# Performance work log

Hardware: AMD Instinct MI355X
Metric: run time of the kernel (lower is better)

Reference implementation:

```python
import jax, jax.numpy as jnp
import numpy as np

B_, L_, DM, DI, DS, DTR, DC = 1, 2048, 2048, 4096, 16, 128, 4


def setup_inputs() -> dict:
    key = jax.random.key(0)
    ks = jax.random.split(key, 8)
    s = lambda k, shape, scale: jax.random.normal(k, shape, jnp.float32) * scale
    inp = {
        "hidden_states": s(ks[0], (B_, L_, DM), 1.0),
        "in_proj_weight": s(ks[1], (2 * DI, DM), DM ** -0.5),
        "conv1d_weight": s(ks[2], (DI, 1, DC), DC ** -0.5),
        "x_proj_weight": s(ks[3], (DTR + 2 * DS, DI), DI ** -0.5),
        "dt_proj_weight": s(ks[4], (DI, DTR), DTR ** -0.5),
        "out_proj_weight": s(ks[5], (DM, DI), DI ** -0.5),
    }
    # dt_proj_bias = inverse-softplus of dt ~ LogUniform[1e-3, 0.1] (as in init_dtprojbias)
    dt = jnp.exp(jax.random.uniform(ks[6], (DI,), jnp.float32) * (np.log(0.1) - np.log(0.001)) + np.log(0.001))
    dt = jnp.clip(dt, 1e-4, None)
    inp["dt_proj_bias"] = dt + jnp.log(-jnp.expm1(-dt))
    # A_log init: log of repeat(arange(1, d_state+1)) per d_inner row
    inp["A_log"] = jnp.log(jnp.tile(jnp.arange(1, DS + 1, dtype=jnp.float32), (DI, 1)))
    inp["D"] = jnp.ones((DI,), jnp.float32)
    return inp


def reference(hidden_states, in_proj_weight, conv1d_weight, x_proj_weight,
              dt_proj_weight, dt_proj_bias, A_log, D, out_proj_weight):
    b, l, dm = hidden_states.shape
    di, ds = A_log.shape
    # in_proj: [b,l,dm] -> xz [b, 2*di, l]
    xz = jnp.einsum('ed,bld->bel', in_proj_weight, hidden_states)
    x, z = xz[:, :di], xz[:, di:]
    # depthwise causal conv1d (pad left d_conv-1, no bias) + SiLU
    x = jax.lax.conv_general_dilated(
        x, conv1d_weight, window_strides=(1,), padding=[(DC - 1, 0)],
        dimension_numbers=('NCH', 'OIH', 'NCH'), feature_group_count=di)
    x = jax.nn.silu(x)  # [b, di, l]
    # x_proj -> dt, B, C
    x_dbl = jnp.einsum('pd,bdl->blp', x_proj_weight, x)  # [b,l,dtr+2*ds]
    dt, Bc, Cc = jnp.split(x_dbl, [DTR, DTR + ds], axis=-1)
    delta = jnp.einsum('dr,blr->bld', dt_proj_weight, dt) + dt_proj_bias
    delta = jax.nn.softplus(delta)  # delta_softplus=True, delta_bias applied
    A = -jnp.exp(A_log)  # [di, ds]
    u = jnp.transpose(x, (0, 2, 1))  # [b,l,di]

    def step(h, inputs):
        d_t, B_t, C_t, u_t = inputs  # [b,di],[b,ds],[b,ds],[b,di]
        dA = jnp.exp(d_t[..., None] * A)                      # [b,di,ds]
        h = h * dA + (d_t * u_t)[..., None] * B_t[:, None, :]  # [b,di,ds]
        y = jnp.einsum('bdn,bn->bd', h, C_t)
        return h, y

    h0 = jnp.zeros((b, di, ds), hidden_states.dtype)
    xs = (jnp.swapaxes(delta, 0, 1), jnp.swapaxes(Bc, 0, 1),
          jnp.swapaxes(Cc, 0, 1), jnp.swapaxes(u, 0, 1))
    _, ys = jax.lax.scan(step, h0, xs)          # [l,b,di]
    y = jnp.swapaxes(ys, 0, 1) + u * D          # skip term u*D
    y = y * jax.nn.silu(jnp.transpose(z, (0, 2, 1)))  # gate
    return jnp.einsum('md,bld->blm', out_proj_weight, y)
```

## Files before the change

kernel.cpp:

```cpp
#include <hip/hip_runtime.h>
#include <hip/hip_bf16.h>

#define LSEQ 2048
#define DMODEL 2048
#define DINNER 4096
#define DSTATE 16
#define DTRANK 128
#define DCONV 4
#define DXP (DTRANK + 2*DSTATE)
#define NCHUNK 64
#define LCHUNK (LSEQ / NCHUNK)
#define KSPLIT 16
#define OKS 4

using bf16 = __hip_bfloat16;
typedef __attribute__((ext_vector_type(8))) short short8;
typedef __attribute__((ext_vector_type(4))) float float4v;

__device__ __forceinline__ float b2f(bf16 v) { return __bfloat162float(v); }
__device__ __forceinline__ bf16 f2b(float v) { return __float2bfloat16(v); }
__device__ __forceinline__ float bl16(unsigned u) { return __uint_as_float(u << 16); }
__device__ __forceinline__ float bh16(unsigned u) { return __uint_as_float(u & 0xffff0000u); }

__device__ __forceinline__ short f2bs(float v) {
    bf16 b = __float2bfloat16(v);
    union { bf16 b; short s; } u; u.b = b; return u.s;
}

__device__ __forceinline__ float fsilu(float x) {
    return x * __builtin_amdgcn_rcpf(1.0f + __expf(-x));
}

__device__ __forceinline__ short8 ld8(const float* p) {
    float4v f0 = *(const float4v*)p;
    float4v f1 = *(const float4v*)(p + 4);
    short8 r;
    r[0] = f2bs(f0[0]); r[1] = f2bs(f0[1]); r[2] = f2bs(f0[2]); r[3] = f2bs(f0[3]);
    r[4] = f2bs(f1[0]); r[5] = f2bs(f1[1]); r[6] = f2bs(f1[2]); r[7] = f2bs(f1[3]);
    return r;
}
__device__ __forceinline__ short8 ld8(const bf16* p) { return *(const short8*)p; }

template<typename CT> __device__ __forceinline__ CT cvtC(float v);
template<> __device__ __forceinline__ bf16  cvtC<bf16>(float v)  { return f2b(v); }
template<> __device__ __forceinline__ float cvtC<float>(float v) { return v; }

template<typename T> __device__ __forceinline__ float cvtL(T v);
template<> __device__ __forceinline__ float cvtL<bf16>(bf16 v)   { return b2f(v); }
template<> __device__ __forceinline__ float cvtL<float>(float v) { return v; }

__device__ __forceinline__ void glds16(const bf16* g, void* lds_base) {
    __builtin_amdgcn_global_load_lds(
        (const __attribute__((address_space(1))) void*)g,
        (__attribute__((address_space(3))) void*)lds_base, 16, 0, 0);
}

__global__ __launch_bounds__(256) void cvt4(
    const float* __restrict__ s0, bf16* __restrict__ d0, int n0,
    const float* __restrict__ s1, bf16* __restrict__ d1, int n1,
    const float* __restrict__ s2, bf16* __restrict__ d2, int n2,
    const float* __restrict__ s3, bf16* __restrict__ d3, int n3)
{
    const int b = blockIdx.x;
    const int nb0 = n0 >> 11, nb1 = n1 >> 11, nb2 = n2 >> 11;
    const float* s; bf16* d; int i;
    if (b < nb0)                  { s = s0; d = d0; i = b * 2048; }
    else if (b < nb0 + nb1)       { s = s1; d = d1; i = (b - nb0) * 2048; }
    else if (b < nb0 + nb1 + nb2) { s = s2; d = d2; i = (b - nb0 - nb1) * 2048; }
    else                          { s = s3; d = d3; i = (b - nb0 - nb1 - nb2) * 2048; }
    i += threadIdx.x * 8;
    *(short8*)(d + i) = ld8(s + i);
}

__global__ __launch_bounds__(256) void cvt1(
    const float* __restrict__ src, bf16* __restrict__ dst, int n)
{
    int i = (blockIdx.x * 256 + threadIdx.x) * 8;
    if (i >= n) return;
    *(short8*)(dst + i) = ld8(src + i);
}

#define GBAR  __builtin_amdgcn_s_barrier()
#define VMW4  asm volatile("s_waitcnt vmcnt(4)" ::: "memory")
#define VMW0  asm volatile("s_waitcnt vmcnt(0)" ::: "memory")

#define LDA8(BASE, RB, AF) do {                                                \
  _Pragma("unroll") for (int mi_ = 0; mi_ < 4; ++mi_)                          \
  _Pragma("unroll") for (int kk_ = 0; kk_ < 2; ++kk_)                          \
    AF[mi_][kk_] = *(const short8*)((BASE) + (((RB) + mi_*16 + t16) << 6)      \
                                    + ((((kk_*4) + quad) ^ sw7) << 3));        \
} while (0)

#define LDB4(BASE, RB, BF) do {                                                \
  _Pragma("unroll") for (int nj_ = 0; nj_ < 2; ++nj_)                          \
  _Pragma("unroll") for (int kk_ = 0; kk_ < 2; ++kk_)                          \
    BF[nj_][kk_] = *(const short8*)((BASE) + (((RB) + nj_*16 + t16) << 6)      \
                                    + ((((kk_*4) + quad) ^ sw7) << 3));        \
} while (0)

#define MM16(AF, BF, MO, NO) do {                                              \
  _Pragma("unroll") for (int kk_ = 0; kk_ < 2; ++kk_)                          \
  _Pragma("unroll") for (int mi_ = 0; mi_ < 4; ++mi_)                          \
  _Pragma("unroll") for (int nj_ = 0; nj_ < 2; ++nj_)                          \
    acc[(MO)+mi_][(NO)+nj_] = __builtin_amdgcn_mfma_f32_16x16x32_bf16(         \
        AF[mi_][kk_], BF[nj_][kk_], acc[(MO)+mi_][(NO)+nj_], 0, 0, 0);         \
} while (0)

#define ST_ALO(tau) do { size_t ko_ = (size_t)(tau) << 6; int bo_ = ((tau)&1) << 15; \
  glds16(sA +       ko_, dA0 + bo_);                                           \
  glds16(sA + oA1 + ko_, dA1 + bo_); } while (0)
#define ST_AHI(tau) do { size_t ko_ = (size_t)(tau) << 6; int bo_ = ((tau)&1) << 15; \
  glds16(sA + oA2 + ko_, dA2 + bo_);                                           \
  glds16(sA + oA3 + ko_, dA3 + bo_); } while (0)
#define ST_BLO(tau) do { size_t ko_ = (size_t)(tau) << 6; int bo_ = ((tau)&1) << 15; \
  glds16(sB +       ko_, dB0 + bo_);                                           \
  glds16(sB + oB1 + ko_, dB1 + bo_); } while (0)
#define ST_BHI(tau) do { size_t ko_ = (size_t)(tau) << 6; int bo_ = ((tau)&1) << 15; \
  glds16(sB + oB2 + ko_, dB2 + bo_);                                           \
  glds16(sB + oB3 + ko_, dB3 + bo_); } while (0)

#define KSTEP(T, BI) do {                                                      \
    const bf16* Ab = As[BI];                                                   \
    const bf16* Bb = Bs[BI];                                                   \
    short8 af[4][2], b0[2][2], b1[2][2];                                       \
                                       \
    LDA8(Ab, wm, af);                                                          \
    LDB4(Bb, wn, b0);                                                          \
    if ((T) + 1 < NT) { ST_AHI((T) + 1); ST_BLO((T) + 1); }                    \
    __builtin_amdgcn_s_setprio(1); MM16(af, b0, 0, 0);                         \
    __builtin_amdgcn_s_setprio(0); GBAR;                                       \
                    \
    LDB4(Bb, wn + 32, b1);                                                     \
    if ((T) + 2 < NT) ST_ALO((T) + 2);                                         \
    __builtin_amdgcn_s_setprio(1); MM16(af, b1, 0, 2);                         \
    __builtin_amdgcn_s_setprio(0); GBAR;                                       \
                           \
    LDA8(Ab, wm + 64, af);                                                     \
    if ((T) + 2 < NT) ST_BHI((T) + 2);                                         \
    __builtin_amdgcn_s_setprio(1); MM16(af, b1, 4, 2);                         \
    __builtin_amdgcn_s_setprio(0); GBAR;                                       \
                                   \
    __builtin_amdgcn_s_setprio(1); MM16(af, b0, 4, 0);                         \
    __builtin_amdgcn_s_setprio(0);                                             \
    if ((T) + 2 < NT) { VMW4; } else { VMW0; }                                 \
    GBAR;                                                                      \
} while (0)

#define GEMM_PRO_COMMON                                                        \
    const int t    = threadIdx.x;                                              \
    const int wave = t >> 6;                                                   \
    const int lane = t & 63;                                                   \
    const int t16  = lane & 15;                                                \
    const int quad = lane >> 4;                                                \
    const int sw7  = t16 & 7;                                                  \
    const int wm   = (wave >> 2) * 128;                                        \
    const int wn   = (wave & 3) * 64;                                          \
    const int lrow  = lane >> 3;                                               \
    const int lseg  = lane & 7;                                                \
    const int segx  = (lseg ^ lrow) * 8;                                       \
    const int bwoff = (wave & 3) * 8 + (wave >> 2) * 64;

#define GEMM_LDS_DSTS                                                          \
    char* dA0 = (char*)&As[0][(  0 + wave * 8) * 64];                          \
    char* dA1 = (char*)&As[0][(128 + wave * 8) * 64];                          \
    char* dA2 = (char*)&As[0][( 64 + wave * 8) * 64];                          \
    char* dA3 = (char*)&As[0][(192 + wave * 8) * 64];                          \
    char* dB0 = (char*)&Bs[0][(  0 + bwoff) * 64];                             \
    char* dB1 = (char*)&Bs[0][(128 + bwoff) * 64];                             \
    char* dB2 = (char*)&Bs[0][( 32 + bwoff) * 64];                             \
    char* dB3 = (char*)&Bs[0][(160 + bwoff) * 64];

__global__ __launch_bounds__(512, 2) void gemm_inproj(
    const bf16* __restrict__ A, int lda,
    const bf16* __restrict__ B, int ldb,
    bf16* __restrict__ C, int ldc, int K)
{
    __shared__ __align__(16) bf16 As[2][256 * 64];
    __shared__ __align__(16) bf16 Bs[2][256 * 64];
    GEMM_PRO_COMMON
    const int bid = blockIdx.x;
    const int s   = (bid & 7) * (gridDim.x >> 3) + (bid >> 3);
    const int bm0 = (s & 7) << 8;
    const int bn0 = (s >> 3) << 8;

    const bf16* sA = A + (size_t)(bm0 + wave * 8 + lrow) * lda + segx;
    const bf16* sB = B + (size_t)(bn0 + bwoff + lrow) * ldb + segx;
    const size_t oA1 = (size_t)128 * lda, oA2 = (size_t)64 * lda, oA3 = (size_t)192 * lda;
    const size_t oB1 = (size_t)128 * ldb, oB2 = (size_t)32 * ldb, oB3 = (size_t)160 * ldb;
    GEMM_LDS_DSTS

    const int NT = K >> 6;

    float4v acc[8][4];
#pragma unroll
    for (int i = 0; i < 8; ++i)
#pragma unroll
        for (int j = 0; j < 4; ++j) acc[i][j] = (float4v)(0.0f);

    ST_ALO(0); ST_AHI(0); ST_BLO(0); ST_BHI(0);
    if (NT > 1) { ST_ALO(1); ST_BHI(1); VMW4; } else { VMW0; }
    GBAR;

    for (int T = 0; T < NT; T += 2) {
        KSTEP(T, 0);
        KSTEP(T + 1, 1);
    }

#pragma unroll
    for (int mi = 0; mi < 8; ++mi) {
#pragma unroll
        for (int nj = 0; nj < 4; ++nj) {
            const int m_base = bm0 + wm + (mi >> 2) * 64 + (mi & 3) * 16 + quad * 4;
            const int n_g    = bn0 + wn + (nj >> 1) * 32 + (nj & 1) * 16 + t16;
#pragma unroll
            for (int r = 0; r < 4; ++r)
                C[(size_t)(m_base + r) * ldc + n_g] = f2b(acc[mi][nj][r]);
        }
    }
}

__global__ __launch_bounds__(512, 2) void gemm_outproj(
    const bf16* __restrict__ A, int lda,
    const bf16* __restrict__ B, int ldb,
    float* __restrict__ P, int ldc, int Kc)
{
    __shared__ __align__(16) bf16 As[2][256 * 64];
    __shared__ __align__(16) bf16 Bs[2][256 * 64];
    GEMM_PRO_COMMON
    const int bid = blockIdx.x;
    const int s   = (bid & 7) * (gridDim.x >> 3) + (bid >> 3);
    const int bm0 = (s & 7) << 8;
    const int t2  = s >> 3;
    const int bn0 = (t2 & 7) << 8;
    const int ks  = t2 >> 3;

    const bf16* sA = A + (size_t)(bm0 + wave * 8 + lrow) * lda + segx + (size_t)ks * Kc;
    const bf16* sB = B + (size_t)(bn0 + bwoff + lrow) * ldb + segx + (size_t)ks * Kc;
    const size_t oA1 = (size_t)128 * lda, oA2 = (size_t)64 * lda, oA3 = (size_t)192 * lda;
    const size_t oB1 = (size_t)128 * ldb, oB2 = (size_t)32 * ldb, oB3 = (size_t)160 * ldb;
    GEMM_LDS_DSTS

    const int NT = Kc >> 6;

    float4v acc[8][4];
#pragma unroll
    for (int i = 0; i < 8; ++i)
#pragma unroll
        for (int j = 0; j < 4; ++j) acc[i][j] = (float4v)(0.0f);

    ST_ALO(0); ST_AHI(0); ST_BLO(0); ST_BHI(0);
    if (NT > 1) { ST_ALO(1); ST_BHI(1); VMW4; } else { VMW0; }
    GBAR;

    for (int T = 0; T < NT; T += 2) {
        KSTEP(T, 0);
        KSTEP(T + 1, 1);
    }

    float* Pk = P + (size_t)ks * 2048 * (size_t)ldc;
#pragma unroll
    for (int mi = 0; mi < 8; ++mi) {
#pragma unroll
        for (int nj = 0; nj < 4; ++nj) {
            const int m_base = bm0 + wm + (mi >> 2) * 64 + (mi & 3) * 16 + quad * 4;
            const int n_g    = bn0 + wn + (nj >> 1) * 32 + (nj & 1) * 16 + t16;
#pragma unroll
            for (int r = 0; r < 4; ++r)
                Pk[(size_t)(m_base + r) * ldc + n_g] = acc[mi][nj][r];
        }
    }
}

__global__ __launch_bounds__(256) void reduce4f(
    const float* __restrict__ P, float* __restrict__ out, int MN)
{
    int i = (blockIdx.x * 256 + threadIdx.x) * 4;
    if (i >= MN) return;
    float4v s = *(const float4v*)(P + i);
#pragma unroll
    for (int ks = 1; ks < OKS; ++ks) {
        float4v v = *(const float4v*)(P + (size_t)ks * MN + i);
#pragma unroll
        for (int j = 0; j < 4; ++j) s[j] += v[j];
    }
    *(float4v*)(out + i) = s;
}

__global__ __launch_bounds__(256) void gemm_xproj(
    const bf16* __restrict__ A, int lda,
    const bf16* __restrict__ B, int ldb,
    float* __restrict__ P)
{
    __shared__ bf16 As[128][64];
    __shared__ bf16 Bs[160][64];

    const int t    = threadIdx.x;
    const int wave = t >> 6;
    const int lane = t & 63;
    const int t16  = lane & 15;
    const int quad = lane >> 4;
    const int wm   = (wave >> 1) * 64;
    const int wn   = (wave & 1) * 80;
    const int bm0  = blockIdx.x * 128;
    const int kbeg = blockIdx.y * (DINNER / KSPLIT);

    const int lrow = lane >> 3;
    const int gseg = ((lane & 7) ^ lrow) * 8;

    const bf16* Ag[4]; char* Ad[4];
#pragma unroll
    for (int g = 0; g < 4; g++) {
        int r = wave * 32 + g * 8;
        Ag[g] = A + (size_t)(bm0 + r + lrow) * lda + gseg + kbeg;
        Ad[g] = (char*)As + r * 128;
    }
    const bf16* Bg[5]; char* Bd[5];
#pragma unroll
    for (int g = 0; g < 5; g++) {
        int r = wave * 40 + g * 8;
        Bg[g] = B + (size_t)(r + lrow) * ldb + gseg + kbeg;
        Bd[g] = (char*)Bs + r * 128;
    }

    float4v acc[4][5];
#pragma unroll
    for (int i = 0; i < 4; i++)
#pragma unroll
        for (int j = 0; j < 5; j++) acc[i][j] = (float4v)(0.0f);

    const int sw = t16 & 7;

    for (int k0 = 0; k0 < DINNER / KSPLIT; k0 += 64) {
        __syncthreads();
#pragma unroll
        for (int g = 0; g < 4; g++) glds16(Ag[g] + k0, Ad[g]);
#pragma unroll
        for (int g = 0; g < 5; g++) glds16(Bg[g] + k0, Bd[g]);
        __syncthreads();

#pragma unroll
        for (int kk = 0; kk < 2; kk++) {
            const int kso = ((kk * 4 + quad) ^ sw) * 8;
            short8 a[4], b[5];
#pragma unroll
            for (int mi = 0; mi < 4; mi++)
                a[mi] = *(const short8*)(&As[wm + mi * 16 + t16][kso]);
#pragma unroll
            for (int nj = 0; nj < 5; nj++)
                b[nj] = *(const short8*)(&Bs[wn + nj * 16 + t16][kso]);
#pragma unroll
            for (int mi = 0; mi < 4; mi++)
#pragma unroll
                for (int nj = 0; nj < 5; nj++)
                    acc[mi][nj] = __builtin_amdgcn_mfma_f32_16x16x32_bf16(
                        a[mi], b[nj], acc[mi][nj], 0, 0, 0);
        }
    }

    float* Pk = P + (size_t)blockIdx.y * LSEQ * DXP;
#pragma unroll
    for (int mi = 0; mi < 4; mi++) {
#pragma unroll
        for (int nj = 0; nj < 5; nj++) {
            int n_g = wn + nj * 16 + t16;
#pragma unroll
            for (int r = 0; r < 4; r++) {
                int m_g = bm0 + wm + mi * 16 + quad * 4 + r;
                Pk[(size_t)m_g * DXP + n_g] = acc[mi][nj][r];
            }
        }
    }
}

template<int BN, typename CT, bool SP>
__global__ __launch_bounds__(256) void gemm_glds64(
    const bf16* __restrict__ A, int lda,
    const bf16* __restrict__ B, int ldb,
    CT* __restrict__ C, int ldc,
    int K, const float* __restrict__ bias)
{
    constexpr int NJ  = BN / 32;
    constexpr int BGL = BN / 32;
    __shared__ bf16 As[128][64];
    __shared__ bf16 Bs[BN][64];

    const int t    = threadIdx.x;
    const int wave = t >> 6;
    const int lane = t & 63;
    const int t16  = lane & 15;
    const int quad = lane >> 4;
    const int wm   = (wave >> 1) * 64;
    const int wn   = (wave & 1) * (BN / 2);
    const int bm0  = blockIdx.x * 128;
    const int bn0  = blockIdx.y * BN;

    const int lrow = lane >> 3;
    const int gseg = (((lane & 7) ^ lrow) * 8);

    const bf16* Ag[4]; char* Ad[4];
#pragma unroll
    for (int g = 0; g < 4; g++) {
        Ag[g] = A + (size_t)(bm0 + wave * 32 + g * 8 + lrow) * lda + gseg;
        Ad[g] = (char*)As + (wave * 32 + g * 8) * 128;
    }
    const bf16* Bg[BGL]; char* Bd[BGL];
#pragma unroll
    for (int g = 0; g < BGL; g++) {
        int r = (BN == 128) ? (wave * 32 + g * 8) : (wave * 16 + g * 8);
        Bg[g] = B + (size_t)(bn0 + r + lrow) * ldb + gseg;
        Bd[g] = (char*)Bs + r * 128;
    }

    float4v acc[4][NJ];
#pragma unroll
    for (int i = 0; i < 4; i++)
#pragma unroll
        for (int j = 0; j < NJ; j++) acc[i][j] = (float4v)(0.0f);

    const int sw = t16 & 7;

    for (int k0 = 0; k0 < K; k0 += 64) {
        __syncthreads();
#pragma unroll
        for (int g = 0; g < 4; g++)   glds16(Ag[g] + k0, Ad[g]);
#pragma unroll
        for (int g = 0; g < BGL; g++) glds16(Bg[g] + k0, Bd[g]);
        __syncthreads();

#pragma unroll
        for (int kk = 0; kk < 2; kk++) {
            const int kso = ((kk * 4 + quad) ^ sw) * 8;
            short8 a[4], b[NJ];
#pragma unroll
            for (int mi = 0; mi < 4; mi++)
                a[mi] = *(const short8*)(&As[wm + mi * 16 + t16][kso]);
#pragma unroll
            for (int nj = 0; nj < NJ; nj++)
                b[nj] = *(const short8*)(&Bs[wn + nj * 16 + t16][kso]);
#pragma unroll
            for (int mi = 0; mi < 4; mi++)
#pragma unroll
                for (int nj = 0; nj < NJ; nj++)
                    acc[mi][nj] = __builtin_amdgcn_mfma_f32_16x16x32_bf16(
                        a[mi], b[nj], acc[mi][nj], 0, 0, 0);
        }
    }

#pragma unroll
    for (int mi = 0; mi < 4; mi++) {
#pragma unroll
        for (int nj = 0; nj < NJ; nj++) {
            int n_g = bn0 + wn + nj * 16 + t16;
            float bia = SP ? bias[n_g] : 0.0f;
#pragma unroll
            for (int r = 0; r < 4; r++) {
                int m_g = bm0 + wm + mi * 16 + quad * 4 + r;
                float v = acc[mi][nj][r];
                if (SP) {
                    float x = v + bia;
                    v = (x > 20.0f) ? x : __logf(1.0f + __expf(x));
                }
                C[(size_t)m_g * ldc + n_g] = cvtC<CT>(v);
            }
        }
    }
}

template<typename AT, typename CT, bool SP>
__global__ __launch_bounds__(256) void gemm_bt(
    const AT* __restrict__ A, int lda,
    const float* __restrict__ B, int ldb,
    CT* __restrict__ C, int ldc,
    int M, int N, int K,
    const float* __restrict__ bias)
{
    __shared__ bf16 As[64][40];
    __shared__ bf16 Bs[64][40];

    const int t    = threadIdx.x;
    const int bm0  = blockIdx.x * 64;
    const int bn0  = blockIdx.y * 64;
    const int row  = t >> 2;
    const int seg  = (t & 3) * 8;
    const int wave = t >> 6;
    const int lane = t & 63;
    const int wm   = (wave >> 1) * 32;
    const int wn   = (wave & 1) * 32;
    const int t16  = lane & 15;
    const int quad = lane >> 4;

    float4v acc[2][2];
#pragma unroll
    for (int i = 0; i < 2; i++)
#pragma unroll
        for (int j = 0; j < 2; j++) acc[i][j] = (float4v)(0.0f);

    const AT*    Aptr = A + (size_t)(bm0 + row) * lda + seg;
    const float* Bptr = B + (size_t)(bn0 + row) * ldb + seg;
    const bool a_ok = (bm0 + row) < M;
    const bool b_ok = (bn0 + row) < N;
    const short8 zero8 = (short8)(0);

    for (int k0 = 0; k0 < K; k0 += 32) {
        short8 av = a_ok ? ld8(Aptr + k0) : zero8;
        short8 bv = b_ok ? ld8(Bptr + k0) : zero8;
        __syncthreads();
        *(short8*)(&As[row][seg]) = av;
        *(short8*)(&Bs[row][seg]) = bv;
        __syncthreads();

        short8 a0 = *(const short8*)(&As[wm + t16][quad * 8]);
        short8 a1 = *(const short8*)(&As[wm + 16 + t16][quad * 8]);
        short8 b0 = *(const short8*)(&Bs[wn + t16][quad * 8]);
        short8 b1 = *(const short8*)(&Bs[wn + 16 + t16][quad * 8]);
        acc[0][0] = __builtin_amdgcn_mfma_f32_16x16x32_bf16(a0, b0, acc[0][0], 0, 0, 0);
        acc[0][1] = __builtin_amdgcn_mfma_f32_16x16x32_bf16(a0, b1, acc[0][1], 0, 0, 0);
        acc[1][0] = __builtin_amdgcn_mfma_f32_16x16x32_bf16(a1, b0, acc[1][0], 0, 0, 0);
        acc[1][1] = __builtin_amdgcn_mfma_f32_16x16x32_bf16(a1, b1, acc[1][1], 0, 0, 0);
    }

#pragma unroll
    for (int i = 0; i < 2; i++) {
#pragma unroll
        for (int j = 0; j < 2; j++) {
            int n_g = bn0 + wn + j * 16 + t16;
            if (n_g >= N) continue;
            float bia = SP ? bias[n_g] : 0.0f;
#pragma unroll
            for (int r = 0; r < 4; r++) {
                int m_g = bm0 + wm + i * 16 + quad * 4 + r;
                if (m_g >= M) continue;
                float v = acc[i][j][r];
                if (SP) {
                    float x = v + bia;
                    v = (x > 20.0f) ? x : log1pf(__expf(x));
                }
                C[(size_t)m_g * ldc + n_g] = cvtC<CT>(v);
            }
        }
    }
}

__global__ __launch_bounds__(256) void reduce_splitk(
    const float* __restrict__ P, bf16* __restrict__ C, float* __restrict__ bc, int MN)
{
    int i = blockIdx.x * 256 + threadIdx.x;
    if (i >= MN) return;
    float s = 0.f;
#pragma unroll
    for (int ks = 0; ks < KSPLIT; ks++) s += P[(size_t)ks * MN + i];
    C[i] = f2b(s);
    int l = i / DXP;
    int p = i - l * DXP;
    if (p >= DTRANK) bc[l * 32 + (p - DTRANK)] = s;
}

__global__ __launch_bounds__(256) void conv_silu_par(
    const bf16* __restrict__ xz, const float* __restrict__ w, bf16* __restrict__ xc)
{
    const int d  = blockIdx.x * 256 + threadIdx.x;
    const int lc = blockIdx.y * 64;
    const float w0 = w[d * 4 + 0];
    const float w1 = w[d * 4 + 1];
    const float w2 = w[d * 4 + 2];
    const float w3 = w[d * 4 + 3];
    const size_t S = 2 * DINNER;
    const bf16* p = xz + d;
    float xm3 = 0.f, xm2 = 0.f, xm1 = 0.f;
    if (lc >= 3) {
        xm3 = b2f(p[(size_t)(lc - 3) * S]);
        xm2 = b2f(p[(size_t)(lc - 2) * S]);
        xm1 = b2f(p[(size_t)(lc - 1) * S]);
    }
    for (int l = lc; l < lc + 64; ++l) {
        float x0 = b2f(p[(size_t)l * S]);
        float a = w0 * xm3 + w1 * xm2 + w2 * xm1 + w3 * x0;
        xc[(size_t)l * DINNER + d] = f2b(fsilu(a));
        xm3 = xm2; xm2 = xm1; xm1 = x0;
    }
}

__global__ __launch_bounds__(256) void conv_silu_inplace(
    bf16* __restrict__ xz, const float* __restrict__ w)
{
    const int d = blockIdx.x * 256 + threadIdx.x;
    const float w0 = w[d * 4 + 0];
    const float w1 = w[d * 4 + 1];
    const float w2 = w[d * 4 + 2];
    const float w3 = w[d * 4 + 3];
    bf16* p = xz + d;
    const size_t S = 2 * DINNER;
    float xm3 = 0.f, xm2 = 0.f, xm1 = 0.f;
    for (int l = 0; l < LSEQ; l += 4) {
        float x0 = b2f(p[(size_t)(l + 0) * S]);
        float x1 = b2f(p[(size_t)(l + 1) * S]);
        float x2 = b2f(p[(size_t)(l + 2) * S]);
        float x3 = b2f(p[(size_t)(l + 3) * S]);
        float a0 = w0 * xm3 + w1 * xm2 + w2 * xm1 + w3 * x0;
        float a1 = w0 * xm2 + w1 * xm1 + w2 * x0  + w3 * x1;
        float a2 = w0 * xm1 + w1 * x0  + w2 * x1  + w3 * x2;
        float a3 = w0 * x0  + w1 * x1  + w2 * x2  + w3 * x3;
        p[(size_t)(l + 0) * S] = f2b(a0 / (1.0f + __expf(-a0)));
        p[(size_t)(l + 1) * S] = f2b(a1 / (1.0f + __expf(-a1)));
        p[(size_t)(l + 2) * S] = f2b(a2 / (1.0f + __expf(-a2)));
        p[(size_t)(l + 3) * S] = f2b(a3 / (1.0f + __expf(-a3)));
        xm3 = x1; xm2 = x2; xm1 = x3;
    }
}

__global__ __launch_bounds__(256) void scan_chunk1(
    const float* __restrict__ dlt, const bf16* __restrict__ xc,
    const float* __restrict__ bc, const float* __restrict__ A_log,
    float* __restrict__ hend, float* __restrict__ Pbuf)
{
    const int d = blockIdx.x * 256 + threadIdx.x;
    const int c = blockIdx.y;

    float Ac[16];
    {
        const float* ap = A_log + d * DSTATE;
#pragma unroll
        for (int i = 0; i < 16; i++) Ac[i] = -__expf(ap[i]);
    }

    float h[16];
#pragma unroll
    for (int i = 0; i < 16; i++) h[i] = 0.f;
    float sdelta = 0.f;

    const float* pd = dlt + (size_t)c * LCHUNK * DINNER + d;
    const bf16*  pu = xc  + (size_t)c * LCHUNK * DINNER + d;
    const float* pb = bc  + (size_t)c * LCHUNK * 32;

#pragma unroll 2
    for (int l = 0; l < LCHUNK; ++l) {
        const float delta = *pd;
        const float u     = b2f(*pu);
        const float du    = delta * u;
        sdelta += delta;
        float4v B0 = *(const float4v*)pb;
        float4v B1 = *(const float4v*)(pb + 4);
        float4v B2 = *(const float4v*)(pb + 8);
        float4v B3 = *(const float4v*)(pb + 12);
#pragma unroll
        for (int i = 0; i < 16; i++) {
            float dA = __expf(delta * Ac[i]);
            float Bi = (i < 4) ? B0[i] : (i < 8) ? B1[i - 4] : (i < 12) ? B2[i - 8] : B3[i - 12];
            h[i] = h[i] * dA + du * Bi;
        }
        pd += DINNER; pu += DINNER; pb += 32;
    }

    float* hp = hend + ((size_t)c * DINNER + d) * DSTATE;
    float* pp = Pbuf + ((size_t)c * DINNER + d) * DSTATE;
#pragma unroll
    for (int q = 0; q < 4; q++) {
        float4v hv, pv;
#pragma unroll
        for (int j = 0; j < 4; j++) {
            hv[j] = h[q * 4 + j];
            pv[j] = __expf(sdelta * Ac[q * 4 + j]);
        }
        *(float4v*)(hp + q * 4) = hv;
        *(float4v*)(pp + q * 4) = pv;
    }
}

__global__ __launch_bounds__(256) void scan_combine(
    float* __restrict__ hend, const float* __restrict__ Pbuf)
{
    const int dn = blockIdx.x * 256 + threadIdx.x;
    const size_t STR = (size_t)DINNER * DSTATE;
    float H = 0.f;
    size_t idx = dn;
    for (int c0 = 0; c0 < NCHUNK; c0 += 8) {
        float he[8], pp[8];
#pragma unroll
        for (int j = 0; j < 8; j++) {
            he[j] = hend[idx + (size_t)j * STR];
            pp[j] = Pbuf[idx + (size_t)j * STR];
        }
#pragma unroll
        for (int j = 0; j < 8; j++) {
            hend[idx + (size_t)j * STR] = H;
            H = he[j] + pp[j] * H;
        }
        idx += 8 * STR;
    }
}

__global__ __launch_bounds__(256) void scan_chunk2(
    const float* __restrict__ dlt, const bf16* __restrict__ xc,
    bf16* __restrict__ xz, const float* __restrict__ bc,
    const float* __restrict__ A_log, const float* __restrict__ Dp,
    const float* __restrict__ Hin)
{
    const int d = blockIdx.x * 256 + threadIdx.x;
    const int c = blockIdx.y;

    float Ac[16];
    {
        const float* ap = A_log + d * DSTATE;
#pragma unroll
        for (int i = 0; i < 16; i++) Ac[i] = -__expf(ap[i]);
    }
    const float Dv = Dp[d];

    float h[16];
    {
        const float* hp = Hin + ((size_t)c * DINNER + d) * DSTATE;
#pragma unroll
        for (int q = 0; q < 4; q++) {
            float4v hv = *(const float4v*)(hp + q * 4);
#pragma unroll
            for (int j = 0; j < 4; j++) h[q * 4 + j] = hv[j];
        }
    }

    const float* pd = dlt + (size_t)c * LCHUNK * DINNER + d;
    const bf16*  pu = xc  + (size_t)c * LCHUNK * DINNER + d;
    const float* pb = bc  + (size_t)c * LCHUNK * 32;
    bf16*        pz = xz  + (size_t)c * LCHUNK * (2 * DINNER) + DINNER + d;

#pragma unroll 2
    for (int l = 0; l < LCHUNK; ++l) {
        const float delta = *pd;
        const float u     = b2f(*pu);
        const float du    = delta * u;
        float4v B0 = *(const float4v*)pb;
        float4v B1 = *(const float4v*)(pb + 4);
        float4v B2 = *(const float4v*)(pb + 8);
        float4v B3 = *(const float4v*)(pb + 12);
        float4v C0 = *(const float4v*)(pb + 16);
        float4v C1 = *(const float4v*)(pb + 20);
        float4v C2 = *(const float4v*)(pb + 24);
        float4v C3 = *(const float4v*)(pb + 28);
        float yv = 0.f;
#pragma unroll
        for (int i = 0; i < 16; i++) {
            float dA = __expf(delta * Ac[i]);
            float Bi = (i < 4) ? B0[i] : (i < 8) ? B1[i - 4] : (i < 12) ? B2[i - 8] : B3[i - 12];
            float Ci = (i < 4) ? C0[i] : (i < 8) ? C1[i - 4] : (i < 12) ? C2[i - 8] : C3[i - 12];
            h[i] = h[i] * dA + du * Bi;
            yv += h[i] * Ci;
        }
        yv += u * Dv;
        float z = b2f(*pz);
        yv *= fsilu(z);
        *pz = f2b(yv);
        pd += DINNER; pu += DINNER; pb += 32; pz += 2 * DINNER;
    }
}

template<typename DT>
__global__ __launch_bounds__(256) void scan_serial(
    const DT* __restrict__ dlt, bf16* __restrict__ xz,
    const bf16* __restrict__ xdbl,
    const float* __restrict__ A_log, const float* __restrict__ Dp)
{
    const int nq = threadIdx.x & 3;
    const int d  = blockIdx.x * 64 + (threadIdx.x >> 2);
    float Ac[4];
#pragma unroll
    for (int i = 0; i < 4; i++)
        Ac[i] = -__expf(A_log[d * DSTATE + nq * 4 + i]);
    const float Dv = Dp[d];
    float h[4] = {0.f, 0.f, 0.f, 0.f};
    for (int l = 0; l < LSEQ; ++l) {
        const float delta = cvtL<DT>(dlt[(size_t)l * DINNER + d]);
        const float u     = b2f(xz[(size_t)l * (2 * DINNER) + d]);
        const uint2 qb = *(const uint2*)(xdbl + (size_t)l * DXP + DTRANK + nq * 4);
        const uint2 qc = *(const uint2*)(xdbl + (size_t)l * DXP + DTRANK + DSTATE + nq * 4);
        float Bv[4] = { bl16(qb.x), bh16(qb.x), bl16(qb.y), bh16(qb.y) };
        float Cv[4] = { bl16(qc.x), bh16(qc.x), bl16(qc.y), bh16(qc.y) };
        const float du = delta * u;
        float yv = 0.f;
#pragma unroll
        for (int i = 0; i < 4; i++) {
            float dA = __expf(delta * Ac[i]);
            h[i] = h[i] * dA + du * Bv[i];
            yv += h[i] * Cv[i];
        }
        yv += __shfl_xor(yv, 1);
        yv += __shfl_xor(yv, 2);
        if (nq == 0) {
            yv += u * Dv;
            bf16* zp = xz + (size_t)l * (2 * DINNER) + DINNER + d;
            float z = b2f(*zp);
            yv *= z / (1.0f + __expf(-z));
            *zp = f2b(yv);
        }
    }
}

extern "C" void kernel_launch(void* const* d_in, const int* in_sizes, int n_in,
                              void* d_out, int out_size, void* d_ws, size_t ws_size,
                              hipStream_t stream)
{
    const float* hs      = (const float*)d_in[0];
    const float* w_in    = (const float*)d_in[1];
    const float* w_conv  = (const float*)d_in[2];
    const float* w_xproj = (const float*)d_in[3];
    const float* w_dt    = (const float*)d_in[4];
    const float *w_out, *b_dt, *A_log, *Dp;
    if (in_sizes[5] == DMODEL * DINNER) {
        w_out = (const float*)d_in[5];
        b_dt  = (const float*)d_in[6];
        A_log = (const float*)d_in[7];
        Dp    = (const float*)d_in[8];
    } else {
        b_dt  = (const float*)d_in[5];
        A_log = (const float*)d_in[6];
        Dp    = (const float*)d_in[7];
        w_out = (const float*)d_in[8];
    }
    float* out = (float*)d_out;

    const size_t SZ_XZ   = (size_t)LSEQ * 2 * DINNER * sizeof(bf16);
    const size_t SZ_XC   = (size_t)LSEQ * DINNER * sizeof(bf16);
    const size_t SZ_XDBL = (size_t)LSEQ * DXP * sizeof(bf16);
    const size_t SZ_DLTF = (size_t)LSEQ * DINNER * sizeof(float);
    const size_t SZ_HP   = (size_t)NCHUNK * DINNER * DSTATE * sizeof(float);
    const size_t SZ_BC   = (size_t)LSEQ * 32 * sizeof(float);

    char* p = (char*)d_ws;
    bf16* xz = (bf16*)p; p += SZ_XZ;

    const size_t need_fast = SZ_XZ + SZ_XC + SZ_XDBL + SZ_DLTF + 2 * SZ_HP + SZ_BC;
    const bool fast = ws_size >= need_fast;

    dim3 blk(256);

    if (fast) {
        bf16*  xc   = (bf16*)p;  p += SZ_XC;
        bf16*  xdbl = (bf16*)p;  p += SZ_XDBL;
        char*  hpr  = p;         p += SZ_DLTF;
        char*  dreg = p;
        float* dlt  = (float*)hpr;
        float* hend = (float*)dreg;
        float* Pbuf = (float*)(dreg + SZ_HP);
        float* bcb  = (float*)(dreg + 2 * SZ_HP);

        bf16*  w_in_b  = (bf16*)hpr;
        float* xp_part = (float*)hpr;
        bf16*  hs_b    = (bf16*)dreg;
        bf16*  w_dt_b  = (bf16*)(dreg + (size_t)LSEQ * DMODEL * sizeof(bf16));
        bf16*  w_xp_b  = (bf16*)(dreg + (size_t)LSEQ * DMODEL * sizeof(bf16)
                                      + (size_t)DINNER * DTRANK * sizeof(bf16));
        bf16*  w_out_b = (bf16*)xc;
        float* p_out   = (float*)hpr;

        {
            int n0 = 2 * DINNER * DMODEL, n1 = LSEQ * DMODEL;
            int n2 = DINNER * DTRANK,     n3 = DXP * DINNER;
            cvt4<<<dim3((n0 + n1 + n2 + n3) / 2048), blk, 0, stream>>>(
                w_in, w_in_b, n0, hs, hs_b, n1, w_dt, w_dt_b, n2, w_xproj, w_xp_b, n3);
        }

        gemm_inproj<<<dim3(256), dim3(512), 0, stream>>>(
            hs_b, DMODEL, w_in_b, DMODEL, xz, 2*DINNER, DMODEL);

        conv_silu_par<<<dim3(DINNER/256, LSEQ/64), blk, 0, stream>>>(xz, w_conv, xc);

        gemm_xproj<<<dim3(LSEQ/128, KSPLIT), blk, 0, stream>>>(
            xc, DINNER, w_xp_b, DINNER, xp_part);
        reduce_splitk<<<dim3((LSEQ * DXP + 255) / 256), blk, 0, stream>>>(
            xp_part, xdbl, bcb, LSEQ * DXP);

        gemm_glds64<128, float, true><<<dim3(LSEQ/128, DINNER/128), blk, 0, stream>>>(
            xdbl, DXP, w_dt_b, DTRANK, dlt, DINNER, DTRANK, b_dt);

        scan_chunk1<<<dim3(DINNER/256, NCHUNK), blk, 0, stream>>>(
            dlt, xc, bcb, A_log, hend, Pbuf);
        scan_combine<<<dim3(DINNER*DSTATE/256), blk, 0, stream>>>(hend, Pbuf);
        scan_chunk2<<<dim3(DINNER/256, NCHUNK), blk, 0, stream>>>(
            dlt, xc, xz, bcb, A_log, Dp, hend);

        cvt1<<<dim3((DMODEL*DINNER)/2048), blk, 0, stream>>>(w_out, w_out_b, DMODEL*DINNER);
        gemm_outproj<<<dim3(256), dim3(512), 0, stream>>>(
            xz + DINNER, 2*DINNER, w_out_b, DINNER, p_out, DMODEL, DINNER/OKS);
        reduce4f<<<dim3(LSEQ*DMODEL/1024), blk, 0, stream>>>(
            p_out, out, LSEQ*DMODEL);
    } else {
        bf16* xdbl = (bf16*)p; p += SZ_XDBL;
        size_t used = (size_t)(p - (char*)d_ws);
        bool dlt_f32 = (ws_size - used) >= SZ_DLTF;

        gemm_bt<float, bf16, false><<<dim3(LSEQ/64, (2*DINNER)/64), blk, 0, stream>>>(
            hs, DMODEL, w_in, DMODEL, xz, 2*DINNER, LSEQ, 2*DINNER, DMODEL, nullptr);
        conv_silu_inplace<<<dim3(DINNER/256), blk, 0, stream>>>(xz, w_conv);
        gemm_bt<bf16, bf16, false><<<dim3(LSEQ/64, 3), blk, 0, stream>>>(
            xz, 2*DINNER, w_xproj, DINNER, xdbl, DXP, LSEQ, DXP, DINNER, nullptr);
        if (dlt_f32) {
            float* dlt = (float*)p;
            gemm_bt<bf16, float, true><<<dim3(LSEQ/64, DINNER/64), blk, 0, stream>>>(
                xdbl, DXP, w_dt, DTRANK, dlt, DINNER, LSEQ, DINNER, DTRANK, b_dt);
            scan_serial<float><<<dim3(DINNER/64), blk, 0, stream>>>(dlt, xz, xdbl, A_log, Dp);
        } else {
            bf16* dlt = (bf16*)p;
            gemm_bt<bf16, bf16, true><<<dim3(LSEQ/64, DINNER/64), blk, 0, stream>>>(
                xdbl, DXP, w_dt, DTRANK, dlt, DINNER, LSEQ, DINNER, DTRANK, b_dt);
            scan_serial<bf16><<<dim3(DINNER/64), blk, 0, stream>>>(dlt, xz, xdbl, A_log, Dp);
        }
        gemm_bt<bf16, float, false><<<dim3(LSEQ/64, DMODEL/64), blk, 0, stream>>>(
            xz + DINNER, 2*DINNER, w_out, DINNER, out, DMODEL, LSEQ, DMODEL, DINNER, nullptr);
    }
}
```

Baseline: 401.2 us.

## Replace split-K out_proj GEMM with single-pass 128x128 tile kernel

```diff
diff --git a/kernel.cpp b/kernel.cpp
--- a/kernel.cpp
+++ b/kernel.cpp
@@ -11,7 +11,6 @@
 #define NCHUNK 64
 #define LCHUNK (LSEQ / NCHUNK)
 #define KSPLIT 16
-#define OKS 4
 
 using bf16 = __hip_bfloat16;
 typedef __attribute__((ext_vector_type(8))) short short8;
@@ -219,71 +218,93 @@
     }
 }
 
-__global__ __launch_bounds__(512, 2) void gemm_outproj(
+__global__ __launch_bounds__(256) void gemm_outproj(
     const bf16* __restrict__ A, int lda,
     const bf16* __restrict__ B, int ldb,
-    float* __restrict__ P, int ldc, int Kc)
-{
-    __shared__ __align__(16) bf16 As[2][256 * 64];
-    __shared__ __align__(16) bf16 Bs[2][256 * 64];
-    GEMM_PRO_COMMON
+    float* __restrict__ C, int ldc, int K)
+{
+    __shared__ bf16 As[128][64];
+    __shared__ bf16 Bs[128][64];
+
+    const int t    = threadIdx.x;
+    const int wave = t >> 6;
+    const int lane = t & 63;
+    const int t16  = lane & 15;
+    const int quad = lane >> 4;
+    const int wm   = (wave >> 1) * 64;
+    const int wn   = (wave & 1) * 64;
+
     const int bid = blockIdx.x;
-    const int s   = (bid & 7) * (gridDim.x >> 3) + (bid >> 3);
-    const int bm0 = (s & 7) << 8;
-    const int t2  = s >> 3;
-    const int bn0 = (t2 & 7) << 8;
-    const int ks  = t2 >> 3;
-
-    const bf16* sA = A + (size_t)(bm0 + wave * 8 + lrow) * lda + segx + (size_t)ks * Kc;
-    const bf16* sB = B + (size_t)(bn0 + bwoff + lrow) * ldb + segx + (size_t)ks * Kc;
-    const size_t oA1 = (size_t)128 * lda, oA2 = (size_t)64 * lda, oA3 = (size_t)192 * lda;
-    const size_t oB1 = (size_t)128 * ldb, oB2 = (size_t)32 * ldb, oB3 = (size_t)160 * ldb;
-    GEMM_LDS_DSTS
-
-    const int NT = Kc >> 6;
-
-    float4v acc[8][4];
-#pragma unroll
-    for (int i = 0; i < 8; ++i)
-#pragma unroll
-        for (int j = 0; j < 4; ++j) acc[i][j] = (float4v)(0.0f);
-
-    ST_ALO(0); ST_AHI(0); ST_BLO(0); ST_BHI(0);
-    if (NT > 1) { ST_ALO(1); ST_BHI(1); VMW4; } else { VMW0; }
-    GBAR;
-
-    for (int T = 0; T < NT; T += 2) {
-        KSTEP(T, 0);
-        KSTEP(T + 1, 1);
-    }
-
-    float* Pk = P + (size_t)ks * 2048 * (size_t)ldc;
-#pragma unroll
-    for (int mi = 0; mi < 8; ++mi) {
-#pragma unroll
-        for (int nj = 0; nj < 4; ++nj) {
-            const int m_base = bm0 + wm + (mi >> 2) * 64 + (mi & 3) * 16 + quad * 4;
-            const int n_g    = bn0 + wn + (nj >> 1) * 32 + (nj & 1) * 16 + t16;
-#pragma unroll
-            for (int r = 0; r < 4; ++r)
-                Pk[(size_t)(m_base + r) * ldc + n_g] = acc[mi][nj][r];
-        }
-    }
-}
-
-__global__ __launch_bounds__(256) void reduce4f(
-    const float* __restrict__ P, float* __restrict__ out, int MN)
-{
-    int i = (blockIdx.x * 256 + threadIdx.x) * 4;
-    if (i >= MN) return;
-    float4v s = *(const float4v*)(P + i);
-#pragma unroll
-    for (int ks = 1; ks < OKS; ++ks) {
-        float4v v = *(const float4v*)(P + (size_t)ks * MN + i);
-#pragma unroll
-        for (int j = 0; j < 4; ++j) s[j] += v[j];
-    }
-    *(float4v*)(out + i) = s;
+    const int m_t = ((bid & 1) << 3) | ((bid >> 3) & 7);
+    const int n_t = (((bid >> 1) & 3) << 2) | ((bid >> 6) & 3);
+    const int bm0 = m_t << 7;
+    const int bn0 = n_t << 7;
+
+    const int lrow = lane >> 3;
+    const int gseg = ((lane & 7) ^ lrow) * 8;
+
+    const bf16* Ag[4]; char* Ad[4];
+#pragma unroll
+    for (int g = 0; g < 4; g++) {
+        int r = wave * 32 + g * 8;
+        Ag[g] = A + (size_t)(bm0 + r + lrow) * lda + gseg;
+        Ad[g] = (char*)As + r * 128;
+    }
+    const bf16* Bg[4]; char* Bd[4];
+#pragma unroll
+    for (int g = 0; g < 4; g++) {
+        int r = wave * 32 + g * 8;
+        Bg[g] = B + (size_t)(bn0 + r + lrow) * ldb + gseg;
+        Bd[g] = (char*)Bs + r * 128;
+    }
+
+    float4v acc[4][4];
+#pragma unroll
+    for (int i = 0; i < 4; i++)
+#pragma unroll
+        for (int j = 0; j < 4; j++) acc[i][j] = (float4v)(0.0f);
+
+    const int sw = t16 & 7;
+
+    for (int k0 = 0; k0 < K; k0 += 64) {
+        __syncthreads();
+#pragma unroll
+        for (int g = 0; g < 4; g++) glds16(Ag[g] + k0, Ad[g]);
+#pragma unroll
+        for (int g = 0; g < 4; g++) glds16(Bg[g] + k0, Bd[g]);
+        __syncthreads();
+
+#pragma unroll
+        for (int kk = 0; kk < 2; kk++) {
+            const int kso = ((kk * 4 + quad) ^ sw) * 8;
+            short8 a[4], b[4];
+#pragma unroll
+            for (int mi = 0; mi < 4; mi++)
+                a[mi] = *(const short8*)(&As[wm + mi * 16 + t16][kso]);
+#pragma unroll
+            for (int nj = 0; nj < 4; nj++)
+                b[nj] = *(const short8*)(&Bs[wn + nj * 16 + t16][kso]);
+#pragma unroll
+            for (int mi = 0; mi < 4; mi++)
+#pragma unroll
+                for (int nj = 0; nj < 4; nj++)
+                    acc[mi][nj] = __builtin_amdgcn_mfma_f32_16x16x32_bf16(
+                        a[mi], b[nj], acc[mi][nj], 0, 0, 0);
+        }
+    }
+
+#pragma unroll
+    for (int mi = 0; mi < 4; mi++) {
+#pragma unroll
+        for (int nj = 0; nj < 4; nj++) {
+            int n_g = bn0 + wn + nj * 16 + t16;
+#pragma unroll
+            for (int r = 0; r < 4; r++) {
+                int m_g = bm0 + wm + mi * 16 + quad * 4 + r;
+                C[(size_t)m_g * ldc + n_g] = acc[mi][nj][r];
+            }
+        }
+    }
 }
 
 __global__ __launch_bounds__(256) void gemm_xproj(
@@ -848,7 +869,6 @@
         bf16*  w_xp_b  = (bf16*)(dreg + (size_t)LSEQ * DMODEL * sizeof(bf16)
                                       + (size_t)DINNER * DTRANK * sizeof(bf16));
         bf16*  w_out_b = (bf16*)xc;
-        float* p_out   = (float*)hpr;
 
         {
             int n0 = 2 * DINNER * DMODEL, n1 = LSEQ * DMODEL;
@@ -877,10 +897,8 @@
             dlt, xc, xz, bcb, A_log, Dp, hend);
 
         cvt1<<<dim3((DMODEL*DINNER)/2048), blk, 0, stream>>>(w_out, w_out_b, DMODEL*DINNER);
-        gemm_outproj<<<dim3(256), dim3(512), 0, stream>>>(
-            xz + DINNER, 2*DINNER, w_out_b, DINNER, p_out, DMODEL, DINNER/OKS);
-        reduce4f<<<dim3(LSEQ*DMODEL/1024), blk, 0, stream>>>(
-            p_out, out, LSEQ*DMODEL);
+        gemm_outproj<<<dim3(256), blk, 0, stream>>>(
+            xz + DINNER, 2*DINNER, w_out_b, DINNER, out, DMODEL, DINNER);
     } else {
         bf16* xdbl = (bf16*)p; p += SZ_XDBL;
         size_t used = (size_t)(p - (char*)d_ws);
```

Result: slower. 413.0 us (+3.0%).
